# Performance work log

Measured on AMD Instinct MI355X. Metric: run time of the kernel, lower is better.

The kernel has to match this reference:

```python
import jax, jax.numpy as jnp
import numpy as np

D_MODEL = 1024
N_HEADS = 16
N_KV_HEADS = 4
HEAD_DIM = D_MODEL // N_HEADS
NUM_REP = N_HEADS // N_KV_HEADS
B, T = 2, 2048


def setup_inputs() -> dict:
    key = jax.random.key(0)
    ks = jax.random.split(key, 9)
    s = 0.02
    x = jax.random.normal(ks[0], (B, T, D_MODEL), dtype=jnp.float32)
    # causal mask: True = masked (matches torch masked_fill semantics)
    mask = jnp.triu(jnp.ones((T, T), dtype=bool), k=1)[None, None]
    kv_dim = N_KV_HEADS * HEAD_DIM
    return {
        "x": x,
        "mask": mask,
        "Wq": jax.random.normal(ks[1], (D_MODEL, D_MODEL), jnp.float32) * s,
        "bq": jnp.zeros((D_MODEL,), jnp.float32),
        "Wk": jax.random.normal(ks[2], (D_MODEL, kv_dim), jnp.float32) * s,
        "bk": jnp.zeros((kv_dim,), jnp.float32),
        "Wv": jax.random.normal(ks[3], (D_MODEL, kv_dim), jnp.float32) * s,
        "bv": jnp.zeros((kv_dim,), jnp.float32),
        "Wo": jax.random.normal(ks[4], (D_MODEL, D_MODEL), jnp.float32) * s,
        "bo": jnp.zeros((D_MODEL,), jnp.float32),
    }


def reference(x, mask, Wq, bq, Wk, bk, Wv, bv, Wo, bo):
    Bx, Tx, C = x.shape
    # projections
    q = (x @ Wq + bq).reshape(Bx, Tx, N_HEADS, HEAD_DIM).transpose(0, 2, 1, 3)  # (B,H,T,D)
    k = (x @ Wk + bk).reshape(Bx, Tx, N_KV_HEADS, HEAD_DIM)
    v = (x @ Wv + bv).reshape(Bx, Tx, N_KV_HEADS, HEAD_DIM)
    # repeat_kv: expand+reshape == repeat along head axis
    k = jnp.repeat(k, NUM_REP, axis=2).transpose(0, 2, 1, 3)  # (B,H,T,D)
    v = jnp.repeat(v, NUM_REP, axis=2).transpose(0, 2, 1, 3)
    scale = 1.0 / jnp.sqrt(jnp.asarray(HEAD_DIM, x.dtype))
    attn = jnp.einsum('bhtd,bhsd->bhts', q, k) * scale  # (B,H,T,T)
    attn = jnp.where(mask, -jnp.inf, attn)
    attn = jax.nn.softmax(attn, axis=-1)
    out = jnp.einsum('bhts,bhsd->bhtd', attn, v)
    out = out.transpose(0, 2, 1, 3).reshape(Bx, Tx, C)
    return out @ Wo + bo
```

## Files before the change

kernel.cpp:

```cpp
#include <hip/hip_runtime.h>
#include <hip/hip_bf16.h>
#include <cmath>
#include <stdint.h>


typedef __attribute__((ext_vector_type(4))) float f32x4;
typedef __attribute__((ext_vector_type(16))) float f32x16;
typedef __attribute__((ext_vector_type(8))) short s16x8;
typedef __attribute__((ext_vector_type(8))) unsigned short u16x8;

#define MFMA32(a, b, c) __builtin_amdgcn_mfma_f32_32x32x16_bf16(a, b, c, 0, 0, 0)

__device__ __forceinline__ unsigned short f2bf(float f) {
    unsigned int u = __float_as_uint(f);
    u += 0x7FFFu + ((u >> 16) & 1u);
    return (unsigned short)(u >> 16);
}

__device__ __forceinline__ unsigned int pktr(float lo, float hi) {
    return __builtin_amdgcn_perm(__float_as_uint(hi), __float_as_uint(lo), 0x07060302u);
}

__device__ __forceinline__ void async16(void* lds, const void* g) {
    __builtin_amdgcn_global_load_lds(
        (const __attribute__((address_space(1))) unsigned int*)g,
        (__attribute__((address_space(3))) unsigned int*)lds, 16, 0, 0);
}

__global__ __launch_bounds__(256) void prep(
        const float* __restrict__ x,
        const float* __restrict__ Wq, const float* __restrict__ Wk,
        const float* __restrict__ Wv, const float* __restrict__ Wo,
        const float* __restrict__ bq, const float* __restrict__ bk,
        const float* __restrict__ bv,
        unsigned short* __restrict__ xb, unsigned short* __restrict__ Wqkv,
        unsigned short* __restrict__ Wot, float* __restrict__ biasq, float qscale) {
    __shared__ unsigned short sx[128 * 72];
    __shared__ float tile[32][33];
    const int bid = blockIdx.x, tid = threadIdx.x;
    if (bid < 512) {
        const int mt = bid >> 4, kt = bid & 15;
#pragma unroll
        for (int i = 0; i < 8; ++i) {
            const int flat = (i * 256 + tid) * 4;
            const int row = flat >> 6, col = flat & 63;
            f32x4 ld = *reinterpret_cast<const f32x4*>(
                &x[(size_t)(mt * 128 + row) * 1024 + kt * 64 + col]);
            unsigned short* d = &sx[row * 72 + col];
            d[0] = f2bf(ld.x); d[1] = f2bf(ld.y); d[2] = f2bf(ld.z); d[3] = f2bf(ld.w);
        }
        __syncthreads();
#pragma unroll
        for (int j = 0; j < 4; ++j) {
            const int idx = j * 256 + tid;
            const int kb = idx >> 7, m = idx & 127;
            u16x8 v = *reinterpret_cast<const u16x8*>(&sx[m * 72 + kb * 8]);
            *reinterpret_cast<u16x8*>(
                &xb[(size_t)(((mt * 16 + kt) * 8 + kb) * 128 + m) * 8]) = v;
        }
    } else if (bid < 3072) {
        int id = bid - 512;
        const float* W; unsigned short* out; int N, nbase; float scale = 1.0f;
        if (id < 1024)      { W = Wq; out = Wqkv; N = 1024; nbase = 0;    scale = qscale; }
        else if (id < 1280) { W = Wk; out = Wqkv; N = 256;  nbase = 1024; id -= 1024; }
        else if (id < 1536) { W = Wv; out = Wqkv; N = 256;  nbase = 1280; id -= 1280; }
        else                { W = Wo; out = Wot;  N = 1024; nbase = 0;    id -= 1536; }
        const int nb = N >> 5;
        const int n0 = (id % nb) * 32, k0 = (id / nb) * 32;
        const int tx = tid & 31, ty = tid >> 5;
#pragma unroll
        for (int r = 0; r < 4; ++r)
            tile[ty + r * 8][tx] = W[(size_t)(k0 + ty + r * 8) * N + n0 + tx];
        __syncthreads();
        const int k = k0 + tx;
#pragma unroll
        for (int r = 0; r < 4; ++r) {
            const int n = nbase + n0 + ty + r * 8;
            size_t addr = (size_t)((n >> 6) * 16 + (k >> 6)) * 4096
                        + (size_t)((((k >> 3) & 7) * 64 + (n & 63)) * 8 + (k & 7));
            out[addr] = f2bf(tile[tx][ty + r * 8] * scale);
        }
    } else {
        const int i = (bid - 3072) * 256 + tid;
        if (i < 1024) biasq[i] = bq[i] * qscale;
        else if (i < 1280) biasq[i] = bk[i - 1024];
        else biasq[i] = bv[i - 1280];
    }
}

template <int EPI>
__global__ __launch_bounds__(256) void gemm_mn(
        const unsigned short* __restrict__ A, const unsigned short* __restrict__ Bt,
        const float* __restrict__ bias,
        unsigned short* __restrict__ oQ, unsigned short* __restrict__ oK,
        unsigned short* __restrict__ oV, float* __restrict__ oF) {
    __shared__ alignas(16) unsigned short smem[24576];
    const int tid = threadIdx.x;
    const int lane = tid & 63, w = tid >> 6;
    const int l31 = lane & 31, grp = lane >> 5;
    const int m0 = blockIdx.y * 128, n0 = blockIdx.x * 64;
    const int wm = w * 32;

    const unsigned short* Abase = A + (size_t)blockIdx.y * (16 * 8192) + (size_t)tid * 8;
    const unsigned short* Bbase = Bt + (size_t)blockIdx.x * (16 * 4096) + (size_t)tid * 8;

    f32x16 acc0 = {}, acc1 = {};

#pragma unroll
    for (int i = 0; i < 4; ++i)
        async16(&smem[(size_t)(i * 256 + (tid & 192)) * 8], Abase + (size_t)i * 2048);
#pragma unroll
    for (int i = 0; i < 2; ++i)
        async16(&smem[16384 + (size_t)(i * 256 + (tid & 192)) * 8], Bbase + (size_t)i * 2048);

    for (int kt = 0; kt < 16; ++kt) {
        const int cur = kt & 1;
        unsigned short* cA = smem + cur * 8192;
        unsigned short* cB = smem + 16384 + cur * 4096;
        __syncthreads();
        if (kt < 15) {
            unsigned short* nA = smem + (cur ^ 1) * 8192;
            unsigned short* nB = smem + 16384 + (cur ^ 1) * 4096;
            const unsigned short* ab = Abase + (size_t)(kt + 1) * 8192;
            const unsigned short* bb = Bbase + (size_t)(kt + 1) * 4096;
#pragma unroll
            for (int i = 0; i < 4; ++i)
                async16(&nA[(size_t)(i * 256 + (tid & 192)) * 8], ab + (size_t)i * 2048);
#pragma unroll
            for (int i = 0; i < 2; ++i)
                async16(&nB[(size_t)(i * 256 + (tid & 192)) * 8], bb + (size_t)i * 2048);
        }
#pragma unroll
        for (int kc = 0; kc < 4; ++kc) {
            const int kb = kc * 2 + grp;
            s16x8 a  = *reinterpret_cast<const s16x8*>(&cA[(size_t)(kb * 128 + wm + l31) * 8]);
            s16x8 b0 = *reinterpret_cast<const s16x8*>(&cB[(size_t)(kb * 64 + l31) * 8]);
            s16x8 b1 = *reinterpret_cast<const s16x8*>(&cB[(size_t)(kb * 64 + 32 + l31) * 8]);
            acc0 = MFMA32(a, b0, acc0);
            acc1 = MFMA32(a, b1, acc1);
        }
    }
    const float bv0 = bias[n0 + l31], bv1 = bias[n0 + 32 + l31];
    if (EPI == 0 && n0 >= 1280) {
        __syncthreads();
        const int kvh = (n0 - 1280) >> 6;
#pragma unroll
        for (int r = 0; r < 16; ++r) {
            const int m = wm + (r & 3) + 8 * (r >> 2) + 4 * grp;
            smem[(size_t)l31 * 136 + m] = f2bf(acc0[r] + bv0);
            smem[(size_t)(l31 + 32) * 136 + m] = f2bf(acc1[r] + bv1);
        }
        __syncthreads();
        const int b = m0 >> 11, c0 = (m0 & 2047) >> 6;
        unsigned short* vb = oV + (size_t)((b * 4 + kvh) * 32 + c0) * 4096;
#pragma unroll
        for (int i = 0; i < 4; ++i) {
            const int id = i * 256 + tid;
            const int d = id >> 4, mc = id & 15;
            u16x8 v = *reinterpret_cast<const u16x8*>(&smem[(size_t)d * 136 + mc * 8]);
            *reinterpret_cast<u16x8*>(&vb[(size_t)(mc >> 3) * 4096
                + ((size_t)(mc & 7) * 64 + d) * 8]) = v;
        }
        return;
    }
    if (EPI == 0 && n0 >= 1024) {
        __syncthreads();
        const int kvh = (n0 - 1024) >> 6;
#pragma unroll
        for (int r = 0; r < 16; ++r) {
            const int m = wm + (r & 3) + 8 * (r >> 2) + 4 * grp;
            smem[(size_t)m * 72 + l31] = f2bf(acc0[r] + bv0);
            smem[(size_t)m * 72 + 32 + l31] = f2bf(acc1[r] + bv1);
        }
        __syncthreads();
        const int b = m0 >> 11, c0 = (m0 & 2047) >> 6;
        unsigned short* kb_o = oK + (size_t)((b * 4 + kvh) * 32 + c0) * 4096;
#pragma unroll
        for (int i = 0; i < 4; ++i) {
            const int id = i * 256 + tid;
            const int si = id >> 3, dc = id & 7;
            u16x8 v = *reinterpret_cast<const u16x8*>(&smem[(size_t)si * 72 + dc * 8]);
            *reinterpret_cast<u16x8*>(&kb_o[(size_t)(si >> 6) * 4096
                + ((size_t)dc * 64 + (si & 63)) * 8]) = v;
        }
        return;
    }
#pragma unroll
    for (int r = 0; r < 16; ++r) {
        const int row = m0 + wm + (r & 3) + 8 * (r >> 2) + 4 * grp;
        const float v0 = acc0[r] + bv0, v1 = acc1[r] + bv1;
        if (EPI == 0) {
            oQ[(size_t)row * 1024 + n0 + l31] = f2bf(v0);
            oQ[(size_t)row * 1024 + n0 + 32 + l31] = f2bf(v1);
        } else {
            oF[(size_t)row * 1024 + n0 + l31] = v0;
            oF[(size_t)row * 1024 + n0 + 32 + l31] = v1;
        }
    }
}

__global__ __launch_bounds__(128) void flash_attn(
        const unsigned short* __restrict__ Qb, const unsigned short* __restrict__ Ktl,
        const unsigned short* __restrict__ Vtl, unsigned short* __restrict__ Ot) {
    __shared__ float sO[64][33];
    __shared__ float sL[64];
    const int tid = threadIdx.x;
    const int lane = tid & 63, w = tid >> 6;
    const int ln = lane & 31, grp = lane >> 5;
    const int id = blockIdx.x;
    const int kvh = id & 3;
    const int b = (id >> 2) & 1;
    const int h = kvh * 4 + ((id >> 3) & 3);
    const int strip = 63 - (id >> 5);
    const int t0w = strip * 32;
    const int qrow_g = t0w + ln;
    const int nch = (strip >> 1) + 1;

    const unsigned short* Qrow = Qb + (size_t)(b * 2048 + qrow_g) * 1024 + h * 64;
    s16x8 qf[4];
#pragma unroll
    for (int kk = 0; kk < 4; ++kk)
        qf[kk] = *reinterpret_cast<const s16x8*>(Qrow + kk * 16 + grp * 8);

    const unsigned short* Kc = Ktl + (size_t)((b * 4 + kvh) * 32) * 4096
                                   + ((size_t)grp * 64 + ln) * 8;
    const unsigned short* Vc = Vtl + (size_t)((b * 4 + kvh) * 32) * 4096
                                   + ((size_t)grp * 64 + ln) * 8;

    f32x16 o0 = {}, o1 = {};
    float ltot = 0.f;

    for (int c = w; c < nch; c += 2) {
        const int s0 = c * 64;
        const unsigned short* kc = Kc + (size_t)c * 4096;
        const unsigned short* vc = Vc + (size_t)c * 4096;
        s16x8 kf0[4], kf1[4], vf0[4], vf1[4];
#pragma unroll
        for (int kk = 0; kk < 4; ++kk) {
            kf0[kk] = *reinterpret_cast<const s16x8*>(kc + kk * 1024);
            kf1[kk] = *reinterpret_cast<const s16x8*>(kc + kk * 1024 + 256);
        }
#pragma unroll
        for (int kk = 0; kk < 4; ++kk) {
            vf0[kk] = *reinterpret_cast<const s16x8*>(vc + kk * 1024);
            vf1[kk] = *reinterpret_cast<const s16x8*>(vc + kk * 1024 + 256);
        }
        f32x16 st0 = {}, st1 = {};
#pragma unroll
        for (int kk = 0; kk < 4; ++kk) {
            st0 = MFMA32(kf0[kk], qf[kk], st0);
            st1 = MFMA32(kf1[kk], qf[kk], st1);
        }
        if (s0 + 63 > t0w) {
#pragma unroll
            for (int r = 0; r < 16; ++r) {
                const int keyo = s0 + (r & 3) + 8 * (r >> 2) + 4 * grp;
                if (keyo > qrow_g)      st0[r] = -INFINITY;
                if (keyo + 32 > qrow_g) st1[r] = -INFINITY;
            }
        }
        f32x16 p0, p1;
#pragma unroll
        for (int r = 0; r < 16; ++r) {
            p0[r] = __builtin_amdgcn_exp2f(st0[r]);
            p1[r] = __builtin_amdgcn_exp2f(st1[r]);
        }
        float a0 = 0.f, a1 = 0.f, a2 = 0.f, a3 = 0.f;
#pragma unroll
        for (int r = 0; r < 16; r += 2) {
            a0 += p0[r]; a1 += p0[r + 1];
            a2 += p1[r]; a3 += p1[r + 1];
        }
        ltot += (a0 + a1) + (a2 + a3);
#pragma unroll
        for (int kkp = 0; kkp < 4; ++kkp) {
            const f32x16& pm = (kkp < 2) ? p0 : p1;
            const int A4 = 8 * (kkp & 1);
            unsigned int pA0 = pktr(pm[A4 + 0], pm[A4 + 1]);
            unsigned int pA1 = pktr(pm[A4 + 2], pm[A4 + 3]);
            unsigned int pB0 = pktr(pm[A4 + 4], pm[A4 + 5]);
            unsigned int pB1 = pktr(pm[A4 + 6], pm[A4 + 7]);
            unsigned int x0 = (unsigned int)__shfl_xor((int)(grp ? pA0 : pB0), 32, 64);
            unsigned int x1 = (unsigned int)__shfl_xor((int)(grp ? pA1 : pB1), 32, 64);
            union { unsigned int u[4]; s16x8 v; } pf;
            pf.u[0] = grp ? x0 : pA0;
            pf.u[1] = grp ? x1 : pA1;
            pf.u[2] = grp ? pB0 : x0;
            pf.u[3] = grp ? pB1 : x1;
            o0 = MFMA32(pf.v, vf0[kkp], o0);
            o1 = MFMA32(pf.v, vf1[kkp], o1);
        }
    }

    if (w == 1) {
#pragma unroll
        for (int r = 0; r < 16; ++r) {
            sO[lane][r] = o0[r];
            sO[lane][16 + r] = o1[r];
        }
        sL[lane] = ltot;
    }
    __syncthreads();
    if (w == 1) return;
#pragma unroll
    for (int r = 0; r < 16; ++r) {
        o0[r] += sO[lane][r];
        o1[r] += sO[lane][16 + r];
    }
    ltot += sL[lane];

    const float lfull = ltot + __shfl_xor(ltot, 32, 64);
    const float rl = 1.0f / lfull;
    unsigned short* Otb = Ot + (size_t)((b * 16 + (strip >> 2)) * 16 + h) * 8192
                             + (size_t)(ln >> 3) * 1024 + (ln & 7);
#pragma unroll
    for (int r = 0; r < 16; ++r) {
        const int row = (r & 3) + 8 * (r >> 2) + 4 * grp;
        const float rr = __shfl(rl, row, 64);
        const size_t off = (size_t)((strip & 3) * 32 + row) * 8;
        Otb[off]        = f2bf(o0[r] * rr);
        Otb[off + 4096] = f2bf(o1[r] * rr);
    }
}

extern "C" void kernel_launch(void* const* d_in, const int* in_sizes, int n_in,
                              void* d_out, int out_size, void* d_ws, size_t ws_size,
                              hipStream_t stream) {
    const float* x  = (const float*)d_in[0];
    const float* Wq = (const float*)d_in[2];
    const float* bq = (const float*)d_in[3];
    const float* Wk = (const float*)d_in[4];
    const float* bk = (const float*)d_in[5];
    const float* Wv = (const float*)d_in[6];
    const float* bv = (const float*)d_in[7];
    const float* Wo = (const float*)d_in[8];
    const float* bo = (const float*)d_in[9];
    float* out = (float*)d_out;

    char* ws = (char*)d_ws;
    unsigned short* xb    = (unsigned short*)(ws);
    unsigned short* Wqkv  = (unsigned short*)(ws + (8u  << 20));
    unsigned short* Wot   = (unsigned short*)(ws + (12u << 20));
    float*          biasq = (float*)         (ws + (15u << 20));
    unsigned short* Qb    = (unsigned short*)(ws + (16u << 20));
    unsigned short* Ktl   = (unsigned short*)(ws + (24u << 20));
    unsigned short* Vtl   = (unsigned short*)(ws + (26u << 20));
    unsigned short* Otl   = (unsigned short*)(ws + (28u << 20));

    const float qscale = 0.125f * 1.4426950408889634f;

    prep<<<3078, 256, 0, stream>>>(x, Wq, Wk, Wv, Wo, bq, bk, bv,
                                   xb, Wqkv, Wot, biasq, qscale);
    gemm_mn<0><<<dim3(24, 32), 256, 0, stream>>>(xb, Wqkv, biasq, Qb, Ktl, Vtl, nullptr);
    flash_attn<<<2048, 128, 0, stream>>>(Qb, Ktl, Vtl, Otl);
    gemm_mn<1><<<dim3(16, 32), 256, 0, stream>>>(Otl, Wot, bo, nullptr, nullptr, nullptr, out);
}
```

Before: 164.8 us.

## Permute K tile layout to drop P shuffles and split key chunks over four waves

The K-tile writer in the QKV GEMM epilogue now permutes key rows within each 64-row chunk. The QK^T accumulator rows then land in the order the PV MFMA expects for its A operand, so the cross-lane shuffles and selects that rebuilt the P fragments are removed and the causal mask index math is updated to match. Separately, flash attention runs four waves per block instead of two, with each wave taking every fourth key chunk and three partial results reduced through shared memory. This adds parallelism for the long causal strips at the cost of more LDS and a larger final reduction.

```diff
diff --git a/kernel.cpp b/kernel.cpp
--- a/kernel.cpp
+++ b/kernel.cpp
@@ -179,9 +179,12 @@
         for (int i = 0; i < 4; ++i) {
             const int id = i * 256 + tid;
             const int si = id >> 3, dc = id & 7;
+            const int s6 = si & 63;
+            const int g2 = (s6 >> 2) & 3;
+            const int sp = (g2 == 1 || g2 == 2) ? (s6 ^ 12) : s6;
             u16x8 v = *reinterpret_cast<const u16x8*>(&smem[(size_t)si * 72 + dc * 8]);
             *reinterpret_cast<u16x8*>(&kb_o[(size_t)(si >> 6) * 4096
-                + ((size_t)dc * 64 + (si & 63)) * 8]) = v;
+                + ((size_t)dc * 64 + sp) * 8]) = v;
         }
         return;
     }
@@ -199,11 +202,11 @@
     }
 }
 
-__global__ __launch_bounds__(128) void flash_attn(
+__global__ __launch_bounds__(256) void flash_attn(
         const unsigned short* __restrict__ Qb, const unsigned short* __restrict__ Ktl,
         const unsigned short* __restrict__ Vtl, unsigned short* __restrict__ Ot) {
-    __shared__ float sO[64][33];
-    __shared__ float sL[64];
+    __shared__ float sO[3][64][33];
+    __shared__ float sL[3][64];
     const int tid = threadIdx.x;
     const int lane = tid & 63, w = tid >> 6;
     const int ln = lane & 31, grp = lane >> 5;
@@ -230,7 +233,7 @@
     f32x16 o0 = {}, o1 = {};
     float ltot = 0.f;
 
-    for (int c = w; c < nch; c += 2) {
+    for (int c = w; c < nch; c += 4) {
         const int s0 = c * 64;
         const unsigned short* kc = Kc + (size_t)c * 4096;
         const unsigned short* vc = Vc + (size_t)c * 4096;
@@ -254,7 +257,7 @@
         if (s0 + 63 > t0w) {
 #pragma unroll
             for (int r = 0; r < 16; ++r) {
-                const int keyo = s0 + (r & 3) + 8 * (r >> 2) + 4 * grp;
+                const int keyo = s0 + ((r & 8) << 1) + 8 * grp + (r & 7);
                 if (keyo > qrow_g)      st0[r] = -INFINITY;
                 if (keyo + 32 > qrow_g) st1[r] = -INFINITY;
             }
@@ -275,39 +278,36 @@
 #pragma unroll
         for (int kkp = 0; kkp < 4; ++kkp) {
             const f32x16& pm = (kkp < 2) ? p0 : p1;
-            const int A4 = 8 * (kkp & 1);
-            unsigned int pA0 = pktr(pm[A4 + 0], pm[A4 + 1]);
-            unsigned int pA1 = pktr(pm[A4 + 2], pm[A4 + 3]);
-            unsigned int pB0 = pktr(pm[A4 + 4], pm[A4 + 5]);
-            unsigned int pB1 = pktr(pm[A4 + 6], pm[A4 + 7]);
-            unsigned int x0 = (unsigned int)__shfl_xor((int)(grp ? pA0 : pB0), 32, 64);
-            unsigned int x1 = (unsigned int)__shfl_xor((int)(grp ? pA1 : pB1), 32, 64);
+            const int base = 8 * (kkp & 1);
             union { unsigned int u[4]; s16x8 v; } pf;
-            pf.u[0] = grp ? x0 : pA0;
-            pf.u[1] = grp ? x1 : pA1;
-            pf.u[2] = grp ? pB0 : x0;
-            pf.u[3] = grp ? pB1 : x1;
+            pf.u[0] = pktr(pm[base + 0], pm[base + 1]);
+            pf.u[1] = pktr(pm[base + 2], pm[base + 3]);
+            pf.u[2] = pktr(pm[base + 4], pm[base + 5]);
+            pf.u[3] = pktr(pm[base + 6], pm[base + 7]);
             o0 = MFMA32(pf.v, vf0[kkp], o0);
             o1 = MFMA32(pf.v, vf1[kkp], o1);
         }
     }
 
-    if (w == 1) {
-#pragma unroll
-        for (int r = 0; r < 16; ++r) {
-            sO[lane][r] = o0[r];
-            sO[lane][16 + r] = o1[r];
-        }
-        sL[lane] = ltot;
+    if (w) {
+#pragma unroll
+        for (int r = 0; r < 16; ++r) {
+            sO[w - 1][lane][r] = o0[r];
+            sO[w - 1][lane][16 + r] = o1[r];
+        }
+        sL[w - 1][lane] = ltot;
     }
     __syncthreads();
-    if (w == 1) return;
-#pragma unroll
-    for (int r = 0; r < 16; ++r) {
-        o0[r] += sO[lane][r];
-        o1[r] += sO[lane][16 + r];
-    }
-    ltot += sL[lane];
+    if (w) return;
+#pragma unroll
+    for (int j = 0; j < 3; ++j) {
+#pragma unroll
+        for (int r = 0; r < 16; ++r) {
+            o0[r] += sO[j][lane][r];
+            o1[r] += sO[j][lane][16 + r];
+        }
+        ltot += sL[j][lane];
+    }
 
     const float lfull = ltot + __shfl_xor(ltot, 32, 64);
     const float rl = 1.0f / lfull;
@@ -352,6 +352,6 @@
     prep<<<3078, 256, 0, stream>>>(x, Wq, Wk, Wv, Wo, bq, bk, bv,
                                    xb, Wqkv, Wot, biasq, qscale);
     gemm_mn<0><<<dim3(24, 32), 256, 0, stream>>>(xb, Wqkv, biasq, Qb, Ktl, Vtl, nullptr);
-    flash_attn<<<2048, 128, 0, stream>>>(Qb, Ktl, Vtl, Otl);
+    flash_attn<<<2048, 256, 0, stream>>>(Qb, Ktl, Vtl, Otl);
     gemm_mn<1><<<dim3(16, 32), 256, 0, stream>>>(Otl, Wot, bo, nullptr, nullptr, nullptr, out);
 }
```

Result: slower. 173.8 us (+5.5%).

## Permute K key order to drop P shuffles and prefetch next K chunk

Applied to the files above, without the earlier changes.

The K-projection epilogue now writes keys in a permuted order within each 64-key chunk. That permutation makes the MFMA score layout line up with the PV operand layout, so the cross-lane shfl_xor exchange and selects when packing P are removed and the causal mask index formula is updated to match. The attention loop also prefetches the next chunk's K fragments into registers while the current chunk is being computed. The cost is extra register pressure from double-buffered K fragments, and correctness now depends on the permutation matching in both kernels.

```diff
diff --git a/kernel.cpp b/kernel.cpp
--- a/kernel.cpp
+++ b/kernel.cpp
@@ -179,9 +179,12 @@
         for (int i = 0; i < 4; ++i) {
             const int id = i * 256 + tid;
             const int si = id >> 3, dc = id & 7;
+            const int s6 = si & 63;
+            const int g2 = (s6 >> 2) & 3;
+            const int sp = (g2 == 1 || g2 == 2) ? (s6 ^ 12) : s6;
             u16x8 v = *reinterpret_cast<const u16x8*>(&smem[(size_t)si * 72 + dc * 8]);
             *reinterpret_cast<u16x8*>(&kb_o[(size_t)(si >> 6) * 4096
-                + ((size_t)dc * 64 + (si & 63)) * 8]) = v;
+                + ((size_t)dc * 64 + sp) * 8]) = v;
         }
         return;
     }
@@ -230,21 +233,33 @@
     f32x16 o0 = {}, o1 = {};
     float ltot = 0.f;
 
+    s16x8 kf0[4], kf1[4];
+    {
+        const unsigned short* kc = Kc + (size_t)w * 4096;
+#pragma unroll
+        for (int kk = 0; kk < 4; ++kk) {
+            kf0[kk] = *reinterpret_cast<const s16x8*>(kc + kk * 1024);
+            kf1[kk] = *reinterpret_cast<const s16x8*>(kc + kk * 1024 + 256);
+        }
+    }
+
     for (int c = w; c < nch; c += 2) {
         const int s0 = c * 64;
-        const unsigned short* kc = Kc + (size_t)c * 4096;
         const unsigned short* vc = Vc + (size_t)c * 4096;
-        s16x8 kf0[4], kf1[4], vf0[4], vf1[4];
-#pragma unroll
-        for (int kk = 0; kk < 4; ++kk) {
-            kf0[kk] = *reinterpret_cast<const s16x8*>(kc + kk * 1024);
-            kf1[kk] = *reinterpret_cast<const s16x8*>(kc + kk * 1024 + 256);
-        }
+        s16x8 vf0[4], vf1[4];
 #pragma unroll
         for (int kk = 0; kk < 4; ++kk) {
             vf0[kk] = *reinterpret_cast<const s16x8*>(vc + kk * 1024);
             vf1[kk] = *reinterpret_cast<const s16x8*>(vc + kk * 1024 + 256);
         }
+        const int cn = (c + 2 < nch) ? (c + 2) : c;
+        const unsigned short* kn = Kc + (size_t)cn * 4096;
+        s16x8 kn0[4], kn1[4];
+#pragma unroll
+        for (int kk = 0; kk < 4; ++kk) {
+            kn0[kk] = *reinterpret_cast<const s16x8*>(kn + kk * 1024);
+            kn1[kk] = *reinterpret_cast<const s16x8*>(kn + kk * 1024 + 256);
+        }
         f32x16 st0 = {}, st1 = {};
 #pragma unroll
         for (int kk = 0; kk < 4; ++kk) {
@@ -254,7 +269,7 @@
         if (s0 + 63 > t0w) {
 #pragma unroll
             for (int r = 0; r < 16; ++r) {
-                const int keyo = s0 + (r & 3) + 8 * (r >> 2) + 4 * grp;
+                const int keyo = s0 + ((r & 8) << 1) + 8 * grp + (r & 7);
                 if (keyo > qrow_g)      st0[r] = -INFINITY;
                 if (keyo + 32 > qrow_g) st1[r] = -INFINITY;
             }
@@ -275,20 +290,19 @@
 #pragma unroll
         for (int kkp = 0; kkp < 4; ++kkp) {
             const f32x16& pm = (kkp < 2) ? p0 : p1;
-            const int A4 = 8 * (kkp & 1);
-            unsigned int pA0 = pktr(pm[A4 + 0], pm[A4 + 1]);
-            unsigned int pA1 = pktr(pm[A4 + 2], pm[A4 + 3]);
-            unsigned int pB0 = pktr(pm[A4 + 4], pm[A4 + 5]);
-            unsigned int pB1 = pktr(pm[A4 + 6], pm[A4 + 7]);
-            unsigned int x0 = (unsigned int)__shfl_xor((int)(grp ? pA0 : pB0), 32, 64);
-            unsigned int x1 = (unsigned int)__shfl_xor((int)(grp ? pA1 : pB1), 32, 64);
+            const int base = 8 * (kkp & 1);
             union { unsigned int u[4]; s16x8 v; } pf;
-            pf.u[0] = grp ? x0 : pA0;
-            pf.u[1] = grp ? x1 : pA1;
-            pf.u[2] = grp ? pB0 : x0;
-            pf.u[3] = grp ? pB1 : x1;
+            pf.u[0] = pktr(pm[base + 0], pm[base + 1]);
+            pf.u[1] = pktr(pm[base + 2], pm[base + 3]);
+            pf.u[2] = pktr(pm[base + 4], pm[base + 5]);
+            pf.u[3] = pktr(pm[base + 6], pm[base + 7]);
             o0 = MFMA32(pf.v, vf0[kkp], o0);
             o1 = MFMA32(pf.v, vf1[kkp], o1);
+        }
+#pragma unroll
+        for (int kk = 0; kk < 4; ++kk) {
+            kf0[kk] = kn0[kk];
+            kf1[kk] = kn1[kk];
         }
     }
 
```

Result: faster. 160.9 us (median of 2 runs) (-2.4%).
